# Kernel tuning notes

Measured on AMD Instinct MI355X. Metric: run time of the kernel, lower is better.

Reference implementation:

```python
import math
import jax, jax.numpy as jnp
import numpy as np

N_HEADS = 12


def _rel_to_abs(x):
    # x: [b, h, L, 2L-1] relative logits -> [b, h, L, L] absolute-position scores
    b, h, L, _ = x.shape
    x = jnp.pad(x, ((0, 0), (0, 0), (0, 0), (0, 1)))           # [b,h,L,2L]
    xf = x.reshape(b, h, L * 2 * L)
    xf = jnp.pad(xf, ((0, 0), (0, 0), (0, L - 1)))
    return xf.reshape(b, h, L + 1, 2 * L - 1)[:, :, :L, L - 1:]


def _abs_to_rel(x):
    # x: [b, h, L, L] attention weights -> [b, h, L, 2L-1] relative-position weights
    b, h, L, _ = x.shape
    x = jnp.pad(x, ((0, 0), (0, 0), (0, 0), (0, L - 1)))        # [b,h,L,2L-1]
    xf = x.reshape(b, h, L * (2 * L - 1))
    xf = jnp.pad(xf, ((0, 0), (0, 0), (L, 0)))
    return xf.reshape(b, h, L, 2 * L)[:, :, :, 1:]


def _get_relative_embeddings(emb, length):
    # emb: [n_rel, 2*window+1, k] -> [n_rel, 2*length-1, k]
    window = (emb.shape[1] - 1) // 2
    pad_len = max(length - (window + 1), 0)
    start = max(window + 1 - length, 0)
    if pad_len > 0:
        emb = jnp.pad(emb, ((0, 0), (pad_len, pad_len), (0, 0)))
    return emb[:, start:start + 2 * length - 1]


def setup_inputs() -> dict:
    key = jax.random.key(0)
    ks = jax.random.split(key, 8)
    B, C, T, H = 4, 768, 1024, N_HEADS
    K = C // H
    W = 10
    xavier = math.sqrt(2.0 / (C + C))          # xavier_uniform std analogue
    rel_std = K ** (-0.5)
    return {
        "x": jax.random.normal(ks[0], (B, C, T), jnp.float32),
        "c": jax.random.normal(ks[1], (B, C, T), jnp.float32),
        "Wq": jax.random.normal(ks[2], (C, C), jnp.float32) * xavier,
        "bq": jnp.zeros((C,), jnp.float32),
        "Wk": jax.random.normal(ks[3], (C, C), jnp.float32) * xavier,
        "bk": jnp.zeros((C,), jnp.float32),
        "Wv": jax.random.normal(ks[4], (C, C), jnp.float32) * xavier,
        "bv": jnp.zeros((C,), jnp.float32),
        "Wo": jax.random.normal(ks[5], (C, C), jnp.float32) * xavier,
        "bo": jnp.zeros((C,), jnp.float32),
        "emb_rel_k": jax.random.normal(ks[6], (1, 2 * W + 1, K), jnp.float32) * rel_std,
        "emb_rel_v": jax.random.normal(ks[7], (1, 2 * W + 1, K), jnp.float32) * rel_std,
    }


def reference(x, c, Wq, bq, Wk, bk, Wv, bv, Wo, bo, emb_rel_k, emb_rel_v):
    B, C, T = x.shape
    H = N_HEADS
    K = C // H

    def proj(W_, b_, inp):  # Conv1d(kernel=1) == channel-wise linear
        return jnp.einsum('oi,bit->bot', W_, inp) + b_[None, :, None]

    # [B,C,T] -> [B,H,T,K]
    q = proj(Wq, bq, x).reshape(B, H, K, T).transpose(0, 1, 3, 2)
    k = proj(Wk, bk, c).reshape(B, H, K, T).transpose(0, 1, 3, 2)
    v = proj(Wv, bv, c).reshape(B, H, K, T).transpose(0, 1, 3, 2)

    qs = q * (1.0 / math.sqrt(K))
    scores = jnp.einsum('bhtd,bhsd->bhts', qs, k)               # [B,H,T,T]

    # relative key logits via skewing trick
    rel_k = _get_relative_embeddings(emb_rel_k, T)              # [1,2T-1,K]
    rel_logits = jnp.einsum('bhtd,md->bhtm', qs, rel_k[0])      # [B,H,T,2T-1]
    scores = scores + _rel_to_abs(rel_logits)

    # proximal bias: -log(1 + |i - j|)
    r = jnp.arange(T, dtype=scores.dtype)
    scores = scores - jnp.log1p(jnp.abs(r[None, :] - r[:, None]))[None, None]

    p = jax.nn.softmax(scores, axis=-1)
    out = jnp.einsum('bhts,bhsd->bhtd', p, v)                   # [B,H,T,K]

    # relative value contribution
    rel_v = _get_relative_embeddings(emb_rel_v, T)              # [1,2T-1,K]
    out = out + jnp.einsum('bhtm,md->bhtd', _abs_to_rel(p), rel_v[0])

    out = out.transpose(0, 1, 3, 2).reshape(B, C, T)            # [B,C,T]
    return jnp.einsum('oi,bit->bot', Wo, out) + bo[None, :, None]
```

## Files before the change

kernel.cpp:

```cpp
#include <hip/hip_runtime.h>
#include <hip/hip_bf16.h>

using bf16 = __hip_bfloat16;
typedef __attribute__((ext_vector_type(8))) short short8;
typedef __attribute__((ext_vector_type(4))) float f32x4;

static constexpr int C = 768, T = 1024, H = 12, D = 64;

__device__ __forceinline__ f32x4 mfma16(short8 a, short8 b, f32x4 c){
  return __builtin_amdgcn_mfma_f32_16x16x32_bf16(a, b, c, 0, 0, 0);
}

__device__ __forceinline__ void gload16(const void* g, void* l){
  void* gv = const_cast<void*>(g);
  __builtin_amdgcn_global_load_lds((__attribute__((address_space(1))) void*)gv,
                                   (__attribute__((address_space(3))) void*)l, 16, 0, 0);
}

__device__ __forceinline__ float b2f(short s){
  unsigned u = ((unsigned)(unsigned short)s) << 16;
  return __builtin_bit_cast(float, u);
}

__device__ __forceinline__ int cvtpk(float a, float b){
  int r;
  asm("v_cvt_pk_bf16_f32 %0, %1, %2" : "=v"(r) : "v"(a), "v"(b));
  return r;
}

union PkU { int i[4]; short8 v; };

__global__ __launch_bounds__(256) void prep_kernel(const float* __restrict__ xin,
    const float* __restrict__ cin, const float* __restrict__ Wq,
    const float* __restrict__ Wk, const float* __restrict__ Wv,
    const float* __restrict__ Wo, bf16* __restrict__ xo, bf16* __restrict__ co,
    bf16* __restrict__ wq, bf16* __restrict__ wk, bf16* __restrict__ wv,
    bf16* __restrict__ wo){
  const int z = blockIdx.z;
  if (z < 8){
    __shared__ float tile[64][65];
    const int b = z & 3, which = z >> 2;
    const float* in = which ? cin : xin;
    bf16* out = which ? co : xo;
    const int t0 = blockIdx.x*64, c0 = blockIdx.y*64;
    const int u = threadIdx.x & 63, r0 = threadIdx.x >> 6;
    const float* ip = in + ((size_t)b*C + c0)*T + t0;
    #pragma unroll
    for (int i = r0; i < 64; i += 4) tile[i][u] = ip[(size_t)i*T + u];
    __syncthreads();
    bf16* op = out + ((size_t)b*T + t0)*C + c0;
    #pragma unroll
    for (int j = r0; j < 64; j += 4) op[(size_t)j*C + u] = (bf16)tile[u][j];
  } else {
    const int chunk = (z - 8)*192 + blockIdx.y*16 + blockIdx.x;
    const int m = chunk / 576;
    const int off = (chunk % 576)*1024 + threadIdx.x*4;
    const float* in = m==0 ? Wq : m==1 ? Wk : m==2 ? Wv : Wo;
    bf16* out = m==0 ? wq : m==1 ? wk : m==2 ? wv : wo;
    float4 v = *(const float4*)(in + off);
    out[off+0] = (bf16)v.x; out[off+1] = (bf16)v.y;
    out[off+2] = (bf16)v.z; out[off+3] = (bf16)v.w;
  }
}

__global__ __launch_bounds__(256,3) void gemm_qkv(const bf16* __restrict__ xb,
    const bf16* __restrict__ cb, const bf16* __restrict__ wq, const bf16* __restrict__ wk,
    const bf16* __restrict__ wv, const float* __restrict__ bq, const float* __restrict__ bk,
    const float* __restrict__ bv, bf16* __restrict__ qout, bf16* __restrict__ kout,
    bf16* __restrict__ vout){
  const int tid = threadIdx.x, lane = tid & 63, w = tid >> 6;
  const int wr = w >> 1, wc = w & 1, g = lane >> 4, cl = lane & 15;
  const int bz = blockIdx.y, b = bz & 3, mode = bz >> 2;
  const int lb = blockIdx.x;
  int m0, n0;
  if (mode == 2){ m0 = (lb >> 3)*128; n0 = (lb & 7)*128; }
  else          { m0 = (lb & 7)*128;  n0 = (lb >> 3)*128; }
  const bf16* A  = (mode==0) ? xb + (size_t)b*T*C : (mode==1) ? cb + (size_t)b*T*C : wv;
  const bf16* Bp = (mode==2) ? cb + (size_t)b*T*C : (mode==0) ? wq : wk;
  const float* bias = (mode==0) ? bq : (mode==1) ? bk : bv;
  const float scale = (mode==0) ? 0.125f*1.44269504088896f : 1.0f;
  __shared__ bf16 lA[128*64], lB[128*64];
  f32x4 acc[4][4] = {};
  const bf16* Ars = A  + (size_t)m0*768;
  const bf16* Brs = Bp + (size_t)n0*768;
  for (int k0 = 0; k0 < 768; k0 += 64){
    __syncthreads();
    #pragma unroll
    for (int rr = 0; rr < 4; ++rr){
      const int u = rr*256 + tid;
      const int row = u >> 3, cc = u & 7;
      const int src = row*768 + k0 + ((cc ^ (row & 7))*8);
      gload16(Ars + src, &lA[(size_t)u*8]);
      gload16(Brs + src, &lB[(size_t)u*8]);
    }
    __syncthreads();
    #pragma unroll
    for (int kh = 0; kh < 2; ++kh){
      short8 af[4], bfr[4];
      #pragma unroll
      for (int mi = 0; mi < 4; ++mi){
        const int row = wr*64 + mi*16 + cl;
        af[mi] = *(const short8*)&lA[row*64 + (((g + kh*4) ^ (row & 7))*8)];
      }
      #pragma unroll
      for (int ni = 0; ni < 4; ++ni){
        const int row = wc*64 + ni*16 + cl;
        bfr[ni] = *(const short8*)&lB[row*64 + (((g + kh*4) ^ (row & 7))*8)];
      }
      __builtin_amdgcn_s_setprio(1);
      #pragma unroll
      for (int mi = 0; mi < 4; ++mi)
        #pragma unroll
        for (int ni = 0; ni < 4; ++ni)
          acc[mi][ni] = mfma16(af[mi], bfr[ni], acc[mi][ni]);
      __builtin_amdgcn_s_setprio(0);
    }
  }
  #pragma unroll
  for (int mi = 0; mi < 4; ++mi){
    const int mB = m0 + wr*64 + mi*16 + g*4;
    #pragma unroll
    for (int ni = 0; ni < 4; ++ni){
      const int n = n0 + wc*64 + ni*16 + cl;
      #pragma unroll
      for (int r = 0; r < 4; ++r){
        const int m = mB + r;
        float v = acc[mi][ni][r];
        if (mode <= 1){
          v = (v + bias[n]) * scale;
          bf16* outp = mode ? kout : qout;
          outp[(size_t)b*(H*T*D) + (size_t)(n >> 6)*(T*D) + (size_t)m*D + (n & 63)] = (bf16)v;
        } else {
          v += bias[m];
          vout[(size_t)b*(C*T) + (size_t)m*T + n] = (bf16)v;
        }
      }
    }
  }
}

__global__ __launch_bounds__(256,3) void gemm_o(const bf16* __restrict__ wo,
                                                const bf16* __restrict__ attn,
                                                const float* __restrict__ bias,
                                                float* __restrict__ outp){
  const int tid = threadIdx.x, lane = tid & 63, w = tid >> 6;
  const int wr = w >> 1, wc = w & 1, g = lane >> 4, cl = lane & 15;
  const int b = blockIdx.z;
  const int q = blockIdx.y*6 + blockIdx.x;
  const int m0 = (q >> 3)*128, n0 = (q & 7)*128;
  __shared__ bf16 lA[128*64], lB[128*64];
  f32x4 acc[4][4] = {};
  const bf16* Ars = wo + (size_t)m0*768;
  const bf16* Brs = attn + (size_t)b*T*C + (size_t)n0*768;
  for (int k0 = 0; k0 < 768; k0 += 64){
    __syncthreads();
    #pragma unroll
    for (int rr = 0; rr < 4; ++rr){
      const int u = rr*256 + tid;
      const int row = u >> 3, cc = u & 7;
      const int src = row*768 + k0 + ((cc ^ (row & 7))*8);
      gload16(Ars + src, &lA[(size_t)u*8]);
      gload16(Brs + src, &lB[(size_t)u*8]);
    }
    __syncthreads();
    #pragma unroll
    for (int kh = 0; kh < 2; ++kh){
      short8 af[4], bfr[4];
      #pragma unroll
      for (int mi = 0; mi < 4; ++mi){
        const int row = wr*64 + mi*16 + cl;
        af[mi] = *(const short8*)&lA[row*64 + (((g + kh*4) ^ (row & 7))*8)];
      }
      #pragma unroll
      for (int ni = 0; ni < 4; ++ni){
        const int row = wc*64 + ni*16 + cl;
        bfr[ni] = *(const short8*)&lB[row*64 + (((g + kh*4) ^ (row & 7))*8)];
      }
      __builtin_amdgcn_s_setprio(1);
      #pragma unroll
      for (int mi = 0; mi < 4; ++mi)
        #pragma unroll
        for (int ni = 0; ni < 4; ++ni)
          acc[mi][ni] = mfma16(af[mi], bfr[ni], acc[mi][ni]);
      __builtin_amdgcn_s_setprio(0);
    }
  }
  #pragma unroll
  for (int mi = 0; mi < 4; ++mi){
    const int mB = m0 + wr*64 + mi*16 + g*4;
    #pragma unroll
    for (int ni = 0; ni < 4; ++ni){
      const int n = n0 + wc*64 + ni*16 + cl;
      #pragma unroll
      for (int r = 0; r < 4; ++r){
        const int m = mB + r;
        outp[(size_t)b*(C*T) + (size_t)m*T + n] = acc[mi][ni][r] + bias[m];
      }
    }
  }
}

__global__ __launch_bounds__(256,4) void attn_kernel(const bf16* __restrict__ qws,
                                                     const bf16* __restrict__ kws,
                                                     const bf16* __restrict__ vws,
                                                     bf16* __restrict__ aws,
                                                     const float* __restrict__ relk,
                                                     const float* __restrict__ relv){
  const int tid = threadIdx.x, lane = tid & 63, w = tid >> 6;
  const int g = lane >> 4, cl = lane & 15;
  const int i0 = blockIdx.y*64, bh = blockIdx.x;
  const int b = bh / H, h = bh % H;
  const int ql = w*16 + cl;
  const int qt = i0 + ql;

  __shared__ __align__(16) char smem[40960];
  bf16*  lKV   = (bf16*)smem;
  float* bandS = (float*)(smem + 32768);
  bf16*  relkD = (bf16*)(smem + 38144);
  bf16*  lEmb32 = lKV + 4096;
  bf16*  lEV    = lKV;
  bf16*  lQ     = lKV + 3*4096;

  const bf16* qg = qws + ((size_t)bh*T + i0)*D;
  const bf16* kg = kws + (size_t)bh*T*D;
  const bf16* vg = vws + ((size_t)b*C + h*D)*T;

  int kOff[2], vOff[2], qOff[2], dst[2];
  #pragma unroll
  for (int r = 0; r < 2; ++r){
    const int u = r*256 + tid, L = u >> 3, cc = u & 7;
    const int sc8 = (cc ^ (L & 7))*8;
    const int sig = (((L>>4)&1)<<5) | (((L>>2)&3)<<3) | (((L>>5)&1)<<2) | (L&3);
    kOff[r] = sig*64 + sc8;
    vOff[r] = L*T + sc8;
    qOff[r] = L*64 + sc8;
    dst[r]  = u*8;
  }

  #pragma unroll
  for (int r = 0; r < 2; ++r){
    gload16(qg + qOff[r], &lQ[dst[r]]);
    gload16(kg + kOff[r], &lKV[dst[r]]);
    gload16(vg + vOff[r], &lKV[2*4096 + dst[r]]);
  }
  for (int idx = tid; idx < 2048; idx += 256){
    const int row = idx >> 6, col = idx & 63;
    const float v = (row < 21) ? relk[idx] : 0.0f;
    lEmb32[row*64 + (((col >> 3) ^ (row & 7))*8) + (col & 7)] = (bf16)v;
  }
  __syncthreads();

  const short8 aq0 = *(const short8*)&lQ[ql*64 + ((g ^ (ql & 7))*8)];
  const short8 aq1 = *(const short8*)&lQ[ql*64 + (((g + 4) ^ (ql & 7))*8)];

  #pragma unroll
  for (int ni2 = 0; ni2 < 2; ++ni2){
    const int row = ni2*16 + cl;
    short8 e0 = *(const short8*)&lEmb32[row*64 + ((g ^ (row & 7))*8)];
    short8 e1 = *(const short8*)&lEmb32[row*64 + (((g + 4) ^ (row & 7))*8)];
    f32x4 rk = {};
    rk = mfma16(e0, aq0, rk);
    rk = mfma16(e1, aq1, rk);
    #pragma unroll
    for (int rr = 0; rr < 4; ++rr){
      const int ridx = ni2*16 + 4*g + rr;
      if (ridx < 21) relkD[ql*22 + ridx] = (bf16)rk[rr];
    }
  }
  __syncthreads();

  float mreg = -1e30f, lreg = 0.f;
  f32x4 o[4] = {};
  const int koffA[4] = {8*g, 32 + 8*g, 4 + 8*g, 36 + 8*g};

  for (int jt = 0; jt < 16; ++jt){
    const int j0 = jt*64, cur = jt & 1, nxt = cur ^ 1;
    if (jt < 15){
      const int jn = j0 + 64;
      #pragma unroll
      for (int r = 0; r < 2; ++r){
        gload16(kg + jn*64 + kOff[r], &lKV[nxt*4096 + dst[r]]);
        gload16(vg + jn + vOff[r],    &lKV[(2 + nxt)*4096 + dst[r]]);
      }
      asm volatile("s_waitcnt vmcnt(4)" ::: "memory");
    } else {
      asm volatile("s_waitcnt vmcnt(0)" ::: "memory");
    }
    asm volatile("s_barrier" ::: "memory");

    const bf16* Kc = lKV + cur*4096;
    const bf16* Vc = lKV + (2 + cur)*4096;

    f32x4 s[4] = {};
    __builtin_amdgcn_s_setprio(1);
    #pragma unroll
    for (int ni = 0; ni < 4; ++ni){
      const int row = ni*16 + cl;
      short8 k0f = *(const short8*)&Kc[row*64 + ((g ^ (row & 7))*8)];
      s[ni] = mfma16(k0f, aq0, s[ni]);
      short8 k1f = *(const short8*)&Kc[row*64 + (((g + 4) ^ (row & 7))*8)];
      s[ni] = mfma16(k1f, aq1, s[ni]);
    }
    __builtin_amdgcn_s_setprio(0);

    const int dj = j0 - i0;
    if (dj == 0 || dj == 64 || dj == -64){
      #pragma unroll
      for (int ni = 0; ni < 4; ++ni){
        const int ibase = j0 + koffA[ni] - qt;
        #pragma unroll
        for (int r = 0; r < 4; ++r){
          const int dd = ibase + r;
          float v = s[ni][r] - __log2f(fabsf((float)dd) + 1.0f);
          if ((unsigned)(dd + 10) <= 20u){
            v += b2f(*(const short*)&relkD[ql*22 + dd + 10]);
            bandS[ql*21 + dd + 10] = v;
          }
          s[ni][r] = v;
        }
      }
    } else {
      #pragma unroll
      for (int ni = 0; ni < 4; ++ni){
        const float fb = (float)(j0 + koffA[ni] - qt);
        const float x1 = fabsf(fb) + 1.0f;
        const float base = __log2f(x1);
        const float slope = __builtin_copysignf(1.44269504f, fb) *
                            __builtin_amdgcn_rcpf(x1);
        #pragma unroll
        for (int r = 0; r < 4; ++r)
          s[ni][r] -= __builtin_fmaf((float)r, slope, base);
      }
    }

    float m0 = fmaxf(fmaxf(s[0][0], s[0][1]), fmaxf(s[0][2], s[0][3]));
    float m1 = fmaxf(fmaxf(s[1][0], s[1][1]), fmaxf(s[1][2], s[1][3]));
    float m2 = fmaxf(fmaxf(s[2][0], s[2][1]), fmaxf(s[2][2], s[2][3]));
    float m3 = fmaxf(fmaxf(s[3][0], s[3][1]), fmaxf(s[3][2], s[3][3]));
    float mx = fmaxf(fmaxf(m0, m1), fmaxf(m2, m3));
    mx = fmaxf(mx, __shfl_xor(mx, 16));
    mx = fmaxf(mx, __shfl_xor(mx, 32));
    if (!__all(mx <= mreg + 8.0f)){
      const float mn = fmaxf(mreg, mx);
      const float sc = __builtin_amdgcn_exp2f(mreg - mn);
      lreg *= sc;
      #pragma unroll
      for (int di = 0; di < 4; ++di)
        #pragma unroll
        for (int r = 0; r < 4; ++r) o[di][r] *= sc;
      mreg = mn;
    }
    #pragma unroll
    for (int ni = 0; ni < 4; ++ni)
      #pragma unroll
      for (int r = 0; r < 4; ++r)
        s[ni][r] = __builtin_amdgcn_exp2f(s[ni][r] - mreg);

    PkU bf0, bf1;
    bf0.i[0] = cvtpk(s[0][0], s[0][1]); bf0.i[1] = cvtpk(s[0][2], s[0][3]);
    bf0.i[2] = cvtpk(s[2][0], s[2][1]); bf0.i[3] = cvtpk(s[2][2], s[2][3]);
    bf1.i[0] = cvtpk(s[1][0], s[1][1]); bf1.i[1] = cvtpk(s[1][2], s[1][3]);
    bf1.i[2] = cvtpk(s[3][0], s[3][1]); bf1.i[3] = cvtpk(s[3][2], s[3][3]);

    __builtin_amdgcn_s_setprio(1);
    #pragma unroll
    for (int di = 0; di < 4; ++di){
      const int vrow = di*16 + cl;
      short8 a0 = *(const short8*)&Vc[vrow*64 + ((g ^ (vrow & 7))*8)];
      o[di] = mfma16(a0, bf0.v, o[di]);
      short8 a1 = *(const short8*)&Vc[vrow*64 + (((g + 4) ^ (vrow & 7))*8)];
      o[di] = mfma16(a1, bf1.v, o[di]);
    }
    __builtin_amdgcn_s_setprio(0);

    float rs = 0.f;
    #pragma unroll
    for (int ni = 0; ni < 4; ++ni)
      rs += (s[ni][0] + s[ni][1]) + (s[ni][2] + s[ni][3]);
    rs += __shfl_xor(rs, 16);
    rs += __shfl_xor(rs, 32);
    lreg += rs;

    asm volatile("s_barrier" ::: "memory");
  }

  for (int idx = tid; idx < 2048; idx += 256){
    const int d = idx >> 5, c = idx & 31;
    const float v = (c < 21) ? relv[c*64 + d] : 0.0f;
    lEV[d*32 + (((c >> 3) ^ ((d >> 2) & 3))*8) + (c & 7)] = (bf16)v;
  }
  __syncthreads();

  const float invl = 1.0f / lreg;
  float pb[8];
  #pragma unroll
  for (int e = 0; e < 8; ++e){
    const int ddi = 8*g + e;
    float pv = 0.f;
    if (ddi < 21){
      const int j = qt + ddi - 10;
      if (j >= 0 && j < T)
        pv = __builtin_amdgcn_exp2f(bandS[ql*21 + ddi] - mreg) * invl;
    }
    pb[e] = pv;
  }
  PkU bfE;
  bfE.i[0] = cvtpk(pb[0], pb[1]); bfE.i[1] = cvtpk(pb[2], pb[3]);
  bfE.i[2] = cvtpk(pb[4], pb[5]); bfE.i[3] = cvtpk(pb[6], pb[7]);

  bf16* outp = aws + (size_t)(b*T + qt)*C + h*64;
  #pragma unroll
  for (int di = 0; di < 4; ++di){
    const int arow = di*16 + cl;
    short8 aE = *(const short8*)&lEV[arow*32 + ((g ^ ((arow >> 2) & 3))*8)];
    f32x4 z = {};
    f32x4 ba = mfma16(aE, bfE.v, z);
    const int p0 = cvtpk(o[di][0]*invl + ba[0], o[di][1]*invl + ba[1]);
    const int p1 = cvtpk(o[di][2]*invl + ba[2], o[di][3]*invl + ba[3]);
    *(int2*)(outp + di*16 + 4*g) = make_int2(p0, p1);
  }
}

extern "C" void kernel_launch(void* const* d_in, const int* in_sizes, int n_in,
                              void* d_out, int out_size, void* d_ws, size_t ws_size,
                              hipStream_t stream){
  const float* x    = (const float*)d_in[0];
  const float* cin  = (const float*)d_in[1];
  const float* Wq   = (const float*)d_in[2];
  const float* bq   = (const float*)d_in[3];
  const float* Wk   = (const float*)d_in[4];
  const float* bk   = (const float*)d_in[5];
  const float* Wv   = (const float*)d_in[6];
  const float* bv   = (const float*)d_in[7];
  const float* Wo   = (const float*)d_in[8];
  const float* bo   = (const float*)d_in[9];
  const float* relk = (const float*)d_in[10];
  const float* relv = (const float*)d_in[11];

  char* ws = (char*)d_ws;
  constexpr size_t SZ_W = (size_t)768*768*2;
  constexpr size_t SZ_T = (size_t)4*1024*768*2;
  bf16* wq  = (bf16*)(ws + 0*SZ_W);
  bf16* wk  = (bf16*)(ws + 1*SZ_W);
  bf16* wv  = (bf16*)(ws + 2*SZ_W);
  bf16* wo  = (bf16*)(ws + 3*SZ_W);
  bf16* xb  = (bf16*)(ws + 4*SZ_W);
  bf16* cb  = (bf16*)(ws + 4*SZ_W + 1*SZ_T);
  bf16* qws = (bf16*)(ws + 4*SZ_W + 2*SZ_T);
  bf16* kws = (bf16*)(ws + 4*SZ_W + 3*SZ_T);
  bf16* vws = (bf16*)(ws + 4*SZ_W + 4*SZ_T);
  bf16* attn = xb;

  prep_kernel<<<dim3(16,12,20), 256, 0, stream>>>(x, cin, Wq, Wk, Wv, Wo,
                                                  xb, cb, wq, wk, wv, wo);
  gemm_qkv<<<dim3(48,12), 256, 0, stream>>>(xb, cb, wq, wk, wv, bq, bk, bv, qws, kws, vws);
  attn_kernel<<<dim3(48,16), 256, 0, stream>>>(qws, kws, vws, attn, relk, relv);
  gemm_o<<<dim3(6,8,4), 256, 0, stream>>>(wo, attn, bo, (float*)d_out);
}
```

Before: 92.71 us.

## Double-buffer LDS tiles with async prefetch in projection GEMMs

Restructures the QKV and output projection GEMM main loops to use two LDS buffers with K-step 32. The next tile is prefetched via global_load_lds while the current tile feeds the MFMAs, with manual vmcnt waits and barriers. This aims to hide global load latency that the old load-sync-compute loop exposed. In exchange it doubles the barrier count per K, halves work per iteration, and relies on hand-written waitcnt correctness.

```diff
diff --git a/kernel.cpp b/kernel.cpp
--- a/kernel.cpp
+++ b/kernel.cpp
@@ -79,43 +79,63 @@
   const bf16* Bp = (mode==2) ? cb + (size_t)b*T*C : (mode==0) ? wq : wk;
   const float* bias = (mode==0) ? bq : (mode==1) ? bk : bv;
   const float scale = (mode==0) ? 0.125f*1.44269504088896f : 1.0f;
-  __shared__ bf16 lA[128*64], lB[128*64];
+  __shared__ bf16 lA[2][4096], lB[2][4096];
   f32x4 acc[4][4] = {};
   const bf16* Ars = A  + (size_t)m0*768;
   const bf16* Brs = Bp + (size_t)n0*768;
-  for (int k0 = 0; k0 < 768; k0 += 64){
-    __syncthreads();
-    #pragma unroll
-    for (int rr = 0; rr < 4; ++rr){
-      const int u = rr*256 + tid;
-      const int row = u >> 3, cc = u & 7;
-      const int src = row*768 + k0 + ((cc ^ (row & 7))*8);
-      gload16(Ars + src, &lA[(size_t)u*8]);
-      gload16(Brs + src, &lB[(size_t)u*8]);
-    }
-    __syncthreads();
-    #pragma unroll
-    for (int kh = 0; kh < 2; ++kh){
-      short8 af[4], bfr[4];
-      #pragma unroll
-      for (int mi = 0; mi < 4; ++mi){
-        const int row = wr*64 + mi*16 + cl;
-        af[mi] = *(const short8*)&lA[row*64 + (((g + kh*4) ^ (row & 7))*8)];
-      }
-      #pragma unroll
-      for (int ni = 0; ni < 4; ++ni){
-        const int row = wc*64 + ni*16 + cl;
-        bfr[ni] = *(const short8*)&lB[row*64 + (((g + kh*4) ^ (row & 7))*8)];
-      }
-      __builtin_amdgcn_s_setprio(1);
-      #pragma unroll
-      for (int mi = 0; mi < 4; ++mi)
-        #pragma unroll
-        for (int ni = 0; ni < 4; ++ni)
-          acc[mi][ni] = mfma16(af[mi], bfr[ni], acc[mi][ni]);
-      __builtin_amdgcn_s_setprio(0);
-    }
-  }
+
+  int srcOff[2], dstOff[2];
+  #pragma unroll
+  for (int r = 0; r < 2; ++r){
+    const int u = r*256 + tid, row = u >> 2, cc = u & 3;
+    srcOff[r] = row*768 + ((cc ^ (row & 3))*8);
+    dstOff[r] = u*8;
+  }
+  int aAddr[4], bAddr[4];
+  #pragma unroll
+  for (int mi = 0; mi < 4; ++mi){
+    const int rowA = wr*64 + mi*16 + cl;
+    aAddr[mi] = rowA*32 + ((g ^ (rowA & 3))*8);
+    const int rowB = wc*64 + mi*16 + cl;
+    bAddr[mi] = rowB*32 + ((g ^ (rowB & 3))*8);
+  }
+
+  #pragma unroll
+  for (int r = 0; r < 2; ++r){
+    gload16(Ars + srcOff[r], &lA[0][dstOff[r]]);
+    gload16(Brs + srcOff[r], &lB[0][dstOff[r]]);
+  }
+
+  for (int it = 0; it < 24; ++it){
+    const int cur = it & 1, nxt = cur ^ 1;
+    if (it < 23){
+      const int kn = (it + 1)*32;
+      #pragma unroll
+      for (int r = 0; r < 2; ++r){
+        gload16(Ars + kn + srcOff[r], &lA[nxt][dstOff[r]]);
+        gload16(Brs + kn + srcOff[r], &lB[nxt][dstOff[r]]);
+      }
+      asm volatile("s_waitcnt vmcnt(4)" ::: "memory");
+    } else {
+      asm volatile("s_waitcnt vmcnt(0)" ::: "memory");
+    }
+    asm volatile("s_barrier" ::: "memory");
+
+    short8 af[4], bfr[4];
+    #pragma unroll
+    for (int mi = 0; mi < 4; ++mi) af[mi]  = *(const short8*)&lA[cur][aAddr[mi]];
+    #pragma unroll
+    for (int ni = 0; ni < 4; ++ni) bfr[ni] = *(const short8*)&lB[cur][bAddr[ni]];
+    __builtin_amdgcn_s_setprio(1);
+    #pragma unroll
+    for (int mi = 0; mi < 4; ++mi)
+      #pragma unroll
+      for (int ni = 0; ni < 4; ++ni)
+        acc[mi][ni] = mfma16(af[mi], bfr[ni], acc[mi][ni]);
+    __builtin_amdgcn_s_setprio(0);
+    asm volatile("s_barrier" ::: "memory");
+  }
+
   #pragma unroll
   for (int mi = 0; mi < 4; ++mi){
     const int mB = m0 + wr*64 + mi*16 + g*4;
@@ -148,43 +168,63 @@
   const int b = blockIdx.z;
   const int q = blockIdx.y*6 + blockIdx.x;
   const int m0 = (q >> 3)*128, n0 = (q & 7)*128;
-  __shared__ bf16 lA[128*64], lB[128*64];
+  __shared__ bf16 lA[2][4096], lB[2][4096];
   f32x4 acc[4][4] = {};
   const bf16* Ars = wo + (size_t)m0*768;
   const bf16* Brs = attn + (size_t)b*T*C + (size_t)n0*768;
-  for (int k0 = 0; k0 < 768; k0 += 64){
-    __syncthreads();
-    #pragma unroll
-    for (int rr = 0; rr < 4; ++rr){
-      const int u = rr*256 + tid;
-      const int row = u >> 3, cc = u & 7;
-      const int src = row*768 + k0 + ((cc ^ (row & 7))*8);
-      gload16(Ars + src, &lA[(size_t)u*8]);
-      gload16(Brs + src, &lB[(size_t)u*8]);
-    }
-    __syncthreads();
-    #pragma unroll
-    for (int kh = 0; kh < 2; ++kh){
-      short8 af[4], bfr[4];
-      #pragma unroll
-      for (int mi = 0; mi < 4; ++mi){
-        const int row = wr*64 + mi*16 + cl;
-        af[mi] = *(const short8*)&lA[row*64 + (((g + kh*4) ^ (row & 7))*8)];
-      }
-      #pragma unroll
-      for (int ni = 0; ni < 4; ++ni){
-        const int row = wc*64 + ni*16 + cl;
-        bfr[ni] = *(const short8*)&lB[row*64 + (((g + kh*4) ^ (row & 7))*8)];
-      }
-      __builtin_amdgcn_s_setprio(1);
-      #pragma unroll
-      for (int mi = 0; mi < 4; ++mi)
-        #pragma unroll
-        for (int ni = 0; ni < 4; ++ni)
-          acc[mi][ni] = mfma16(af[mi], bfr[ni], acc[mi][ni]);
-      __builtin_amdgcn_s_setprio(0);
-    }
-  }
+
+  int srcOff[2], dstOff[2];
+  #pragma unroll
+  for (int r = 0; r < 2; ++r){
+    const int u = r*256 + tid, row = u >> 2, cc = u & 3;
+    srcOff[r] = row*768 + ((cc ^ (row & 3))*8);
+    dstOff[r] = u*8;
+  }
+  int aAddr[4], bAddr[4];
+  #pragma unroll
+  for (int mi = 0; mi < 4; ++mi){
+    const int rowA = wr*64 + mi*16 + cl;
+    aAddr[mi] = rowA*32 + ((g ^ (rowA & 3))*8);
+    const int rowB = wc*64 + mi*16 + cl;
+    bAddr[mi] = rowB*32 + ((g ^ (rowB & 3))*8);
+  }
+
+  #pragma unroll
+  for (int r = 0; r < 2; ++r){
+    gload16(Ars + srcOff[r], &lA[0][dstOff[r]]);
+    gload16(Brs + srcOff[r], &lB[0][dstOff[r]]);
+  }
+
+  for (int it = 0; it < 24; ++it){
+    const int cur = it & 1, nxt = cur ^ 1;
+    if (it < 23){
+      const int kn = (it + 1)*32;
+      #pragma unroll
+      for (int r = 0; r < 2; ++r){
+        gload16(Ars + kn + srcOff[r], &lA[nxt][dstOff[r]]);
+        gload16(Brs + kn + srcOff[r], &lB[nxt][dstOff[r]]);
+      }
+      asm volatile("s_waitcnt vmcnt(4)" ::: "memory");
+    } else {
+      asm volatile("s_waitcnt vmcnt(0)" ::: "memory");
+    }
+    asm volatile("s_barrier" ::: "memory");
+
+    short8 af[4], bfr[4];
+    #pragma unroll
+    for (int mi = 0; mi < 4; ++mi) af[mi]  = *(const short8*)&lA[cur][aAddr[mi]];
+    #pragma unroll
+    for (int ni = 0; ni < 4; ++ni) bfr[ni] = *(const short8*)&lB[cur][bAddr[ni]];
+    __builtin_amdgcn_s_setprio(1);
+    #pragma unroll
+    for (int mi = 0; mi < 4; ++mi)
+      #pragma unroll
+      for (int ni = 0; ni < 4; ++ni)
+        acc[mi][ni] = mfma16(af[mi], bfr[ni], acc[mi][ni]);
+    __builtin_amdgcn_s_setprio(0);
+    asm volatile("s_barrier" ::: "memory");
+  }
+
   #pragma unroll
   for (int mi = 0; mi < 4; ++mi){
     const int mB = m0 + wr*64 + mi*16 + g*4;
```

Result: slower. 100.0 us (+7.9%).
